# Optimization experiments

Measured on AMD Instinct MI355X. Metric: run time of the kernel, lower is better.

## Reference

```python
import jax, jax.numpy as jnp
import numpy as np

B, C, CI, H, W = 4, 128, 64, 96, 96  # batch, in_channels, inter_channels, spatial
SS = 2                                # sub_sample_factor (maxpool on phi and g)
BN_EPS = 1e-5


def conv1x1(x, w, b):
    # x: [B,C,H,W], w: [O,C], b: [O]
    return jnp.einsum('bchw,oc->bohw', x, w) + b[None, :, None, None]


def maxpool2(x):
    # 2x2 max pool, stride 2. x: [B,C,H,W]
    b, c, h, w = x.shape
    return x.reshape(b, c, h // 2, 2, w // 2, 2).max(axis=(3, 5))


def setup_inputs() -> dict:
    key = jax.random.key(0)
    ks = jax.random.split(key, 12)
    s_in = 1.0 / np.sqrt(C)
    s_ci = 1.0 / np.sqrt(CI)
    return {
        'x':        jax.random.normal(ks[0], (B, C, H, W), jnp.float32),
        'g_w':      jax.random.normal(ks[1], (CI, C), jnp.float32) * s_in,
        'g_b':      jax.random.normal(ks[2], (CI,), jnp.float32) * 0.01,
        'theta_w':  jax.random.normal(ks[3], (CI, C), jnp.float32) * s_in,
        'theta_b':  jax.random.normal(ks[4], (CI,), jnp.float32) * 0.01,
        'phi_w':    jax.random.normal(ks[5], (CI, C), jnp.float32) * s_in,
        'phi_b':    jax.random.normal(ks[6], (CI,), jnp.float32) * 0.01,
        'W_w':      jax.random.normal(ks[7], (C, CI), jnp.float32) * s_ci,
        'W_b':      jax.random.normal(ks[8], (C,), jnp.float32) * 0.01,
        'bn_gamma': jax.random.normal(ks[9], (C,), jnp.float32) * 0.1 + 1.0,
        'bn_beta':  jax.random.normal(ks[10], (C,), jnp.float32) * 0.1,
        'bn_mean':  jax.random.normal(ks[11], (C,), jnp.float32) * 0.1,
        'bn_var':   jax.random.uniform(jax.random.fold_in(key, 99), (C,), jnp.float32, 0.5, 1.5),
    }


def reference(x, g_w, g_b, theta_w, theta_b, phi_w, phi_b, W_w, W_b,
              bn_gamma, bn_beta, bn_mean, bn_var):
    b = x.shape[0]
    # g: conv1x1 -> maxpool(2) -> [B, N_kv, CI]
    g_x = maxpool2(conv1x1(x, g_w, g_b)).reshape(b, CI, -1).transpose(0, 2, 1)
    # theta: conv1x1 -> [B, N_q, CI]
    theta_x = conv1x1(x, theta_w, theta_b).reshape(b, CI, -1).transpose(0, 2, 1)
    # phi: conv1x1 -> maxpool(2) -> [B, CI, N_kv]
    phi_x = maxpool2(conv1x1(x, phi_w, phi_b)).reshape(b, CI, -1)
    # full affinity [B, N_q, N_kv], softmax over keys (embedded_gaussian)
    f = jnp.einsum('bqc,bck->bqk', theta_x, phi_x)
    attn = jax.nn.softmax(f, axis=-1)
    y = jnp.einsum('bqk,bkc->bqc', attn, g_x)            # [B, N_q, CI]
    y = y.transpose(0, 2, 1).reshape(b, CI, H, W)
    # W: conv1x1 (CI -> C) + BatchNorm (inference form) + residual
    W_y = conv1x1(y, W_w, W_b)
    inv = bn_gamma * jax.lax.rsqrt(bn_var + BN_EPS)
    W_y = W_y * inv[None, :, None, None] + (bn_beta - bn_mean * inv)[None, :, None, None]
    return W_y + x
```

## Files before the change

kernel.cpp:

```cpp
#include <hip/hip_runtime.h>
#include <hip/hip_bf16.h>

#define NB 4
#define NC 128
#define NH 96
#define NQ 9216
#define NKV 2304

typedef __bf16 bf8 __attribute__((ext_vector_type(8)));
typedef float f4 __attribute__((ext_vector_type(4)));
typedef unsigned short u16t;
typedef unsigned int u32t;
typedef u32t u32x4 __attribute__((ext_vector_type(4)));
typedef u16t u16x4v __attribute__((ext_vector_type(4)));

static __device__ __forceinline__ u16t f2bf(float f){
  u32t u = __builtin_bit_cast(u32t, f);
  u = (u + 0x7fffu + ((u >> 16) & 1u)) >> 16;
  return (u16t)u;
}
static __device__ __forceinline__ float bf2f(u16t h){
  return __builtin_bit_cast(float, ((u32t)h) << 16);
}

static __device__ __forceinline__ f4 mfma16(bf8 a, bf8 b, f4 c){
  return __builtin_amdgcn_mfma_f32_16x16x32_bf16(a, b, c, 0, 0, 0);
}

#define GLDS16(gp, lp) __builtin_amdgcn_global_load_lds( \
    (const u32t*)(gp), (u32t*)(lp), 16, 0, 0)

__global__ __launch_bounds__(256) void prep_weights(
    const float* __restrict__ g_w, const float* __restrict__ theta_w,
    const float* __restrict__ phi_w, const float* __restrict__ W_w,
    const float* __restrict__ W_b, const float* __restrict__ bn_gamma,
    const float* __restrict__ bn_beta, const float* __restrict__ bn_mean,
    const float* __restrict__ bn_var,
    u16t* __restrict__ wt_theta, u16t* __restrict__ wt_phi,
    u16t* __restrict__ wt_g, u16t* __restrict__ wt_W,
    float* __restrict__ alpha, float* __restrict__ beta2)
{
  int i = blockIdx.x * 256 + threadIdx.x;
  wt_theta[i] = f2bf(theta_w[i]);
  wt_phi[i]   = f2bf(phi_w[i]);
  wt_g[i]     = f2bf(g_w[i]);
  wt_W[i]     = f2bf(W_w[i]);
  if (blockIdx.x == 0 && threadIdx.x < 128){
    int t = threadIdx.x;
    float inv = bn_gamma[t] * rsqrtf(bn_var[t] + 1e-5f);
    alpha[t] = inv;
    beta2[t] = W_b[t]*inv + bn_beta[t] - bn_mean[t]*inv;
  }
}

__global__ __launch_bounds__(256) void conv3_pool(
    const float* __restrict__ x,
    const u16t* __restrict__ wt_theta, const u16t* __restrict__ wt_phi,
    const u16t* __restrict__ wt_g,
    const float* __restrict__ theta_b, const float* __restrict__ phi_b,
    const float* __restrict__ g_b,
    u16t* __restrict__ theta, u16t* __restrict__ phi, u16t* __restrict__ g_t)
{
  __shared__ __align__(16) u16t xt[64][136];
  const int blk = blockIdx.x;
  const int batch = blk / 144;
  const int t144 = blk % 144;
  const int ph = t144 / 3;
  const int pw0 = (t144 % 3) * 16;
  const int t = threadIdx.x;
  const float* xb = x + (size_t)batch * NC * NQ;

  #pragma unroll
  for (int i = 0; i < 8; ++i){
    int slot = i*256 + t;
    int c = slot >> 4;
    int quad = slot & 15;
    int row = quad >> 3, col4 = (quad & 7)*4;
    int q = (ph*2 + row)*NH + pw0*2 + col4;
    float4 v = *(const float4*)&xb[(size_t)c*NQ + q];
    int pl = row*32 + col4;
    u32t lo, hi;
    asm("v_cvt_pk_bf16_f32 %0, %1, %2" : "=v"(lo) : "v"(v.x), "v"(v.y));
    asm("v_cvt_pk_bf16_f32 %0, %1, %2" : "=v"(hi) : "v"(v.z), "v"(v.w));
    xt[pl+0][c] = (u16t)lo;
    xt[pl+1][c] = (u16t)(lo >> 16);
    xt[pl+2][c] = (u16t)hi;
    xt[pl+3][c] = (u16t)(hi >> 16);
  }
  __syncthreads();

  const int w = t >> 6, l = t & 63, lm = l & 15, lg = l >> 4;
  auto PL = [](int pxi){
    return (((pxi>>1)&1) << 5) + 8*(pxi>>4) + 2*((pxi>>2)&3) + (pxi&1);
  };
  auto QROW = [&](int pxi){
    return (ph*2 + ((pxi>>1)&1))*NH + (pw0 + 4*(pxi>>4) + ((pxi>>2)&3))*2 + (pxi&1);
  };
  bf8 a[4];
  #pragma unroll
  for (int k = 0; k < 4; ++k)
    a[k] = *(const bf8*)&xt[PL(w*16 + lm)][k*32 + lg*8];

  const int kvbase = ph*48 + pw0;
  const int kv = kvbase + 4*w + lg;

  f4 Dth[4];
  #pragma unroll
  for (int s = 0; s < 4; ++s){
    float bv = theta_b[s*16 + lm];
    f4 D = {bv, bv, bv, bv};
    #pragma unroll
    for (int k = 0; k < 4; ++k){
      bf8 b = *(const bf8*)&wt_theta[(s*16 + lm)*128 + k*32 + lg*8];
      D = mfma16(a[k], b, D);
    }
    Dth[s] = D;
  }
  {
    u16t* pp = phi + (size_t)batch * NKV * 64;
    #pragma unroll
    for (int s = 0; s < 4; ++s){
      float bv = phi_b[s*16 + lm];
      f4 D = {bv, bv, bv, bv};
      #pragma unroll
      for (int k = 0; k < 4; ++k){
        bf8 b = *(const bf8*)&wt_phi[(s*16 + lm)*128 + k*32 + lg*8];
        D = mfma16(a[k], b, D);
      }
      float mx = fmaxf(fmaxf(D[0], D[1]), fmaxf(D[2], D[3]));
      pp[(size_t)kv*64 + s*16 + lm] = f2bf(mx);
    }
  }
  float gmx[4];
  #pragma unroll
  for (int s = 0; s < 4; ++s){
    float bv = g_b[s*16 + lm];
    f4 D = {bv, bv, bv, bv};
    #pragma unroll
    for (int k = 0; k < 4; ++k){
      bf8 b = *(const bf8*)&wt_g[(s*16 + lm)*128 + k*32 + lg*8];
      D = mfma16(a[k], b, D);
    }
    gmx[s] = fmaxf(fmaxf(D[0], D[1]), fmaxf(D[2], D[3]));
  }

  __syncthreads();
  u16t* tl = &xt[0][0];
  u16t* gl = &xt[0][0] + 4608;
  #pragma unroll
  for (int s = 0; s < 4; ++s){
    #pragma unroll
    for (int r = 0; r < 4; ++r)
      tl[(w*16 + lg*4 + r)*72 + s*16 + lm] = f2bf(Dth[s][r]);
    gl[(s*16 + lm)*20 + 4*w + lg] = f2bf(gmx[s]);
  }
  __syncthreads();
  {
    u16t* th = theta + (size_t)batch * NQ * 64;
    #pragma unroll
    for (int p = 0; p < 2; ++p){
      int slot = t + 256*p;
      int row = slot >> 3, piece = slot & 7;
      int q = QROW(row);
      *(bf8*)&th[(size_t)q*64 + piece*8] = *(const bf8*)&tl[row*72 + piece*8];
    }
  }
  {
    u16t* gt = g_t + (size_t)batch * 64 * NKV;
    int c = t >> 2, L = t & 3;
    int T = (kvbase >> 4) & 3;
    int kvg = kvbase & ~63;
    u16x4v v;
    #pragma unroll
    for (int u = 0; u < 4; ++u) v[u] = gl[c*20 + L*4 + u];
    *(u16x4v*)&gt[(size_t)c*NKV + kvg + (T>>1)*32 + ((T&1)<<2) + L*8] = v;
  }
}


__global__ __launch_bounds__(256) void attn_partial(
    const u16t* __restrict__ theta, const u16t* __restrict__ phi,
    const u16t* __restrict__ g_t,
    u16t* __restrict__ yp_ws, float* __restrict__ sums_ws)
{
  __shared__ __align__(16) char SM[32768];

  const int bid = blockIdx.x;
  const int blkL = (bid & 7)*96 + (bid >> 3);
  const int batch = blkL / 192;
  const int rem = blkL % 192;
  const int qb = (rem >> 1) * 96;
  const int khb = rem & 1;
  const int t = threadIdx.x;
  const int w = t >> 6, l = t & 63, lm = l & 15, lg = l >> 4;
  const int qw = w >> 1, khw = w & 1;

  const u16t* th = theta + ((size_t)batch*NQ + qb)*64;
  bf8 a[3][2];
  #pragma unroll
  for (int mr = 0; mr < 3; ++mr){
    a[mr][0] = *(const bf8*)&th[(qw*48 + mr*16 + lm)*64 + lg*8];
    a[mr][1] = *(const bf8*)&th[(qw*48 + mr*16 + lm)*64 + 32 + lg*8];
  }
  asm volatile("s_waitcnt vmcnt(0)" ::: "memory");

  const char* phc = (const char*)(phi + (size_t)batch*NKV*64);
  const char* gtc = (const char*)(g_t + (size_t)batch*64*NKV);

  auto STAGE = [&](int kt_s, int bufc){
    #pragma unroll
    for (int j = 0; j < 4; ++j){
      int u = w*4 + j;
      int khu = u >> 3, isg = (u >> 2) & 1, sub = u & 3;
      int kb = khb*1152 + khu*576 + kt_s*32;
      char* dst;
      const char* src;
      if (!isg){
        int row = sub*8 + (l >> 3);
        int swz = ((l & 7) ^ (l >> 3)) << 4;
        dst = SM + (khu*2 + bufc)*4096 + sub*1024 + l*16;
        src = phc + (size_t)(kb + row)*128 + swz;
      } else {
        int row = sub*16 + (l >> 2);
        int swz = (((l & 3) ^ ((l >> 2) & 3)) << 4);
        dst = SM + 16384 + (khu*2 + bufc)*4096 + sub*1024 + l*16;
        src = gtc + (size_t)row*(NKV*2) + (size_t)kb*2 + swz;
      }
      GLDS16(src, dst);
    }
  };

  f4 Y[3][4];
  #pragma unroll
  for (int mr = 0; mr < 3; ++mr)
    #pragma unroll
    for (int s = 0; s < 4; ++s)
      Y[mr][s] = f4{0.f, 0.f, 0.f, 0.f};
  float lsum[3] = {0.f, 0.f, 0.f};

  STAGE(0, 0);

  for (int kt = 0; kt < 18; ++kt){
    const int buf = kt & 1;
    __builtin_amdgcn_s_barrier();
    asm volatile("" ::: "memory");
    if (kt < 17){
      STAGE(kt + 1, buf ^ 1);
      asm volatile("s_waitcnt vmcnt(4)" ::: "memory");
    } else {
      asm volatile("s_waitcnt vmcnt(0)" ::: "memory");
    }
    __builtin_amdgcn_s_barrier();
    asm volatile("" ::: "memory");
    __builtin_amdgcn_sched_barrier(0);

    __builtin_amdgcn_s_setprio(1);

    const char* pb = SM + (khw*2 + buf)*4096;
    const char* gb = SM + 16384 + (khw*2 + buf)*4096;
    const int m7 = lm & 7;

    bf8 bp[2][2];
    #pragma unroll
    for (int tt = 0; tt < 2; ++tt){
      int rb = (tt*16 + lm)*128;
      bp[tt][0] = *(const bf8*)(pb + rb + ((lg ^ m7) << 4));
      bp[tt][1] = *(const bf8*)(pb + rb + (((4 + lg) ^ m7) << 4));
    }
    bf8 bg[4];
    #pragma unroll
    for (int s = 0; s < 4; ++s){
      int rb = (s*16 + lm)*64;
      bg[s] = *(const bf8*)(gb + rb + ((lg ^ (lm & 3)) << 4));
    }

    #pragma unroll
    for (int mr = 0; mr < 3; ++mr){
      f4 S[2];
      #pragma unroll
      for (int tt = 0; tt < 2; ++tt){
        f4 z = {0.f, 0.f, 0.f, 0.f};
        z = mfma16(bp[tt][0], a[mr][0], z);
        S[tt] = mfma16(bp[tt][1], a[mr][1], z);
      }
      u32t wq[4];
      #pragma unroll
      for (int tt = 0; tt < 2; ++tt){
        float p0, p1, p2, p3;
        float a0 = fmaf(S[tt][0], 1.44269504f, -43.2808512f);
        float a1 = fmaf(S[tt][1], 1.44269504f, -43.2808512f);
        float a2 = fmaf(S[tt][2], 1.44269504f, -43.2808512f);
        float a3 = fmaf(S[tt][3], 1.44269504f, -43.2808512f);
        asm("v_exp_f32 %0, %1" : "=v"(p0) : "v"(a0));
        asm("v_exp_f32 %0, %1" : "=v"(p1) : "v"(a1));
        asm("v_exp_f32 %0, %1" : "=v"(p2) : "v"(a2));
        asm("v_exp_f32 %0, %1" : "=v"(p3) : "v"(a3));
        lsum[mr] += (p0 + p1) + (p2 + p3);
        asm("v_cvt_pk_bf16_f32 %0, %1, %2" : "=v"(wq[tt*2])   : "v"(p0), "v"(p1));
        asm("v_cvt_pk_bf16_f32 %0, %1, %2" : "=v"(wq[tt*2+1]) : "v"(p2), "v"(p3));
      }
      bf8 pa = __builtin_bit_cast(bf8, u32x4{wq[0], wq[1], wq[2], wq[3]});
      #pragma unroll
      for (int s = 0; s < 4; ++s)
        Y[mr][s] = mfma16(pa, bg[s], Y[mr][s]);
    }
    __builtin_amdgcn_s_setprio(0);
  }

  float sv[3];
  #pragma unroll
  for (int mr = 0; mr < 3; ++mr){
    float s0 = lsum[mr];
    s0 += __shfl_xor(s0, 16);
    s0 += __shfl_xor(s0, 32);
    sv[mr] = s0;
  }

  __syncthreads();
  float (*ypL)[68] = (float (*)[68])SM;
  if (khw == 0){
    #pragma unroll
    for (int mr = 0; mr < 3; ++mr){
      #pragma unroll
      for (int s = 0; s < 4; ++s)
        #pragma unroll
        for (int r = 0; r < 4; ++r)
          ypL[qw*48 + mr*16 + lg*4 + r][s*16 + lm] = Y[mr][s][r];
      if (lg == 0)
        ypL[qw*48 + mr*16 + lm][64] = sv[mr];
    }
  }
  __syncthreads();
  if (khw == 1){
    #pragma unroll
    for (int mr = 0; mr < 3; ++mr){
      #pragma unroll
      for (int s = 0; s < 4; ++s)
        #pragma unroll
        for (int r = 0; r < 4; ++r)
          ypL[qw*48 + mr*16 + lg*4 + r][s*16 + lm] += Y[mr][s][r];
      if (lg == 0)
        ypL[qw*48 + mr*16 + lm][64] += sv[mr];
    }
  }
  __syncthreads();

  u16t* ypg = yp_ws + (size_t)blkL * (96*64);
  float* sg  = sums_ws + (size_t)blkL * 96;
  #pragma unroll
  for (int i = 0; i < 6; ++i){
    int idx = t + 256*i;
    int q = idx >> 4, c4 = (idx & 15)*4;
    u16x4v v;
    #pragma unroll
    for (int j = 0; j < 4; ++j) v[j] = f2bf(ypL[q][c4 + j]);
    *(u16x4v*)&ypg[q*64 + c4] = v;
  }
  if (t < 96) sg[t] = ypL[t][64];
}

__global__ __launch_bounds__(256) void combine_out(
    const u16t* __restrict__ yp_ws, const float* __restrict__ sums_ws,
    const u16t* __restrict__ wt_W,
    const float* __restrict__ alpha, const float* __restrict__ beta2,
    const float* __restrict__ x, float* __restrict__ out)
{
  __shared__ __align__(16) u16t yl[96][72];
  __shared__ __align__(16) float ol[96][131];
  const int bid = blockIdx.x;
  const int blk = (bid & 7)*48 + (bid >> 3);
  const int batch = blk / 96;
  const int qg = blk % 96;
  const int qb = qg * 96;
  const int t = threadIdx.x;
  const int w = t >> 6, l = t & 63, lm = l & 15, lg = l >> 4;

  const u16t* pA = yp_ws + ((size_t)batch*192 + qg*2) * (96*64);
  const u16t* pB = pA + 96*64;
  const float* sA = sums_ws + ((size_t)batch*192 + qg*2) * 96;
  const float* sB = sA + 96;

  #pragma unroll
  for (int i = 0; i < 6; ++i){
    int idx = t + 256*i;
    int q = idx >> 4, c4 = (idx & 15)*4;
    float inv = 1.0f / (sA[q] + sB[q]);
    u16x4v a4 = *(const u16x4v*)&pA[q*64 + c4];
    u16x4v b4 = *(const u16x4v*)&pB[q*64 + c4];
    u16x4v v;
    #pragma unroll
    for (int j = 0; j < 4; ++j)
      v[j] = f2bf((bf2f(a4[j]) + bf2f(b4[j])) * inv);
    *(u16x4v*)&yl[q][c4] = v;
  }
  __syncthreads();

  #pragma unroll
  for (int i = 0; i < 12; ++i){
    int tau = w + 4*i;
    int qt = tau >> 3, ct = tau & 7;
    bf8 ya0 = *(const bf8*)&yl[qt*16 + lm][lg*8];
    bf8 ya1 = *(const bf8*)&yl[qt*16 + lm][32 + lg*8];
    const u16t* wr = wt_W + (ct*16 + lm)*64;
    bf8 b0 = *(const bf8*)&wr[lg*8];
    bf8 b1 = *(const bf8*)&wr[lg*8 + 32];
    f4 z = {0.f, 0.f, 0.f, 0.f};
    z = mfma16(ya0, b0, z);
    z = mfma16(ya1, b1, z);
    #pragma unroll
    for (int r = 0; r < 4; ++r)
      ol[qt*16 + lg*4 + r][ct*16 + lm] = z[r];
  }
  __syncthreads();

  const float* xb = x + (size_t)batch*NC*NQ + qb;
  float* ob = out + (size_t)batch*NC*NQ + qb;
  #pragma unroll
  for (int i = 0; i < 12; ++i){
    int idx = t + 256*i;
    int c = idx / 24, qv = idx % 24;
    float4 xv = *(const float4*)&xb[(size_t)c*NQ + qv*4];
    float al = alpha[c], be = beta2[c];
    float4 ov;
    ov.x = ol[qv*4 + 0][c]*al + be + xv.x;
    ov.y = ol[qv*4 + 1][c]*al + be + xv.y;
    ov.z = ol[qv*4 + 2][c]*al + be + xv.z;
    ov.w = ol[qv*4 + 3][c]*al + be + xv.w;
    *(float4*)&ob[(size_t)c*NQ + qv*4] = ov;
  }
}

extern "C" void kernel_launch(void* const* d_in, const int* in_sizes, int n_in,
                              void* d_out, int out_size, void* d_ws, size_t ws_size,
                              hipStream_t stream)
{
  const float* x       = (const float*)d_in[0];
  const float* g_w     = (const float*)d_in[1];
  const float* g_b     = (const float*)d_in[2];
  const float* theta_w = (const float*)d_in[3];
  const float* theta_b = (const float*)d_in[4];
  const float* phi_w   = (const float*)d_in[5];
  const float* phi_b   = (const float*)d_in[6];
  const float* W_w     = (const float*)d_in[7];
  const float* W_b     = (const float*)d_in[8];
  const float* bn_g    = (const float*)d_in[9];
  const float* bn_b    = (const float*)d_in[10];
  const float* bn_m    = (const float*)d_in[11];
  const float* bn_v    = (const float*)d_in[12];
  float* out = (float*)d_out;

  char* ws = (char*)d_ws;
  size_t off = 0;
  u16t* theta = (u16t*)(ws + off); off += (size_t)NB*NQ*64*2;
  u16t* phi   = (u16t*)(ws + off); off += (size_t)NB*NKV*64*2;
  u16t* g_t   = (u16t*)(ws + off); off += (size_t)NB*64*NKV*2;
  u16t* wt_theta = (u16t*)(ws + off); off += 64*128*2;
  u16t* wt_phi   = (u16t*)(ws + off); off += 64*128*2;
  u16t* wt_g     = (u16t*)(ws + off); off += 64*128*2;
  u16t* wt_W     = (u16t*)(ws + off); off += 128*64*2;
  float* alpha = (float*)(ws + off); off += 128*4;
  float* beta2 = (float*)(ws + off); off += 128*4;
  u16t* yp_ws  = (u16t*)(ws + off); off += (size_t)768*96*64*2;
  float* sums_ws = (float*)(ws + off); off += (size_t)768*96*4;
  if (off > ws_size) return;

  prep_weights<<<32, 256, 0, stream>>>(g_w, theta_w, phi_w, W_w, W_b,
                                       bn_g, bn_b, bn_m, bn_v,
                                       wt_theta, wt_phi, wt_g, wt_W, alpha, beta2);
  conv3_pool<<<576, 256, 0, stream>>>(x, wt_theta, wt_phi, wt_g,
                                      theta_b, phi_b, g_b, theta, phi, g_t);
  attn_partial<<<768, 256, 0, stream>>>(theta, phi, g_t, yp_ws, sums_ws);
  combine_out<<<384, 256, 0, stream>>>(yp_ws, sums_ws, wt_W, alpha, beta2, x, out);
}
```

Measured before the change: 73.59 us.

## Replace block-shared double-buffered KV staging with per-wave private buffers

Each wave now loads its own phi and g tiles into a private LDS region every iteration, so the two block-wide barriers per key tile go away. Within an iteration the QK^T and exp work runs while the g tile is still loading, and the PV MFMAs are reordered to loop over g fragments on the outside. In exchange, the prefetch of the next tile across iterations is lost. Waves that share the same key half now each fetch the same data, which doubles global/L2 load traffic.

```diff
diff --git a/kernel.cpp b/kernel.cpp
--- a/kernel.cpp
+++ b/kernel.cpp
@@ -206,29 +206,8 @@
 
   const char* phc = (const char*)(phi + (size_t)batch*NKV*64);
   const char* gtc = (const char*)(g_t + (size_t)batch*64*NKV);
-
-  auto STAGE = [&](int kt_s, int bufc){
-    #pragma unroll
-    for (int j = 0; j < 4; ++j){
-      int u = w*4 + j;
-      int khu = u >> 3, isg = (u >> 2) & 1, sub = u & 3;
-      int kb = khb*1152 + khu*576 + kt_s*32;
-      char* dst;
-      const char* src;
-      if (!isg){
-        int row = sub*8 + (l >> 3);
-        int swz = ((l & 7) ^ (l >> 3)) << 4;
-        dst = SM + (khu*2 + bufc)*4096 + sub*1024 + l*16;
-        src = phc + (size_t)(kb + row)*128 + swz;
-      } else {
-        int row = sub*16 + (l >> 2);
-        int swz = (((l & 3) ^ ((l >> 2) & 3)) << 4);
-        dst = SM + 16384 + (khu*2 + bufc)*4096 + sub*1024 + l*16;
-        src = gtc + (size_t)row*(NKV*2) + (size_t)kb*2 + swz;
-      }
-      GLDS16(src, dst);
-    }
-  };
+  char* const pbuf = SM + w*8192;
+  char* const gbuf = pbuf + 4096;
 
   f4 Y[3][4];
   #pragma unroll
@@ -238,42 +217,35 @@
       Y[mr][s] = f4{0.f, 0.f, 0.f, 0.f};
   float lsum[3] = {0.f, 0.f, 0.f};
 
-  STAGE(0, 0);
+  const int m7 = lm & 7;
 
   for (int kt = 0; kt < 18; ++kt){
-    const int buf = kt & 1;
-    __builtin_amdgcn_s_barrier();
-    asm volatile("" ::: "memory");
-    if (kt < 17){
-      STAGE(kt + 1, buf ^ 1);
-      asm volatile("s_waitcnt vmcnt(4)" ::: "memory");
-    } else {
-      asm volatile("s_waitcnt vmcnt(0)" ::: "memory");
-    }
-    __builtin_amdgcn_s_barrier();
-    asm volatile("" ::: "memory");
+    const int kb = khb*1152 + khw*576 + kt*32;
+    #pragma unroll
+    for (int sub = 0; sub < 4; ++sub){
+      int row = sub*8 + (l >> 3);
+      int swz = ((l & 7) ^ (l >> 3)) << 4;
+      GLDS16(phc + (size_t)(kb + row)*128 + swz, pbuf + sub*1024 + l*16);
+    }
+    #pragma unroll
+    for (int sub = 0; sub < 4; ++sub){
+      int row = sub*16 + (l >> 2);
+      int swz = (((l & 3) ^ ((l >> 2) & 3)) << 4);
+      GLDS16(gtc + (size_t)row*(NKV*2) + (size_t)kb*2 + swz,
+             gbuf + sub*1024 + l*16);
+    }
+    asm volatile("s_waitcnt vmcnt(4)" ::: "memory");
     __builtin_amdgcn_sched_barrier(0);
-
     __builtin_amdgcn_s_setprio(1);
-
-    const char* pb = SM + (khw*2 + buf)*4096;
-    const char* gb = SM + 16384 + (khw*2 + buf)*4096;
-    const int m7 = lm & 7;
 
     bf8 bp[2][2];
     #pragma unroll
     for (int tt = 0; tt < 2; ++tt){
       int rb = (tt*16 + lm)*128;
-      bp[tt][0] = *(const bf8*)(pb + rb + ((lg ^ m7) << 4));
-      bp[tt][1] = *(const bf8*)(pb + rb + (((4 + lg) ^ m7) << 4));
-    }
-    bf8 bg[4];
-    #pragma unroll
-    for (int s = 0; s < 4; ++s){
-      int rb = (s*16 + lm)*64;
-      bg[s] = *(const bf8*)(gb + rb + ((lg ^ (lm & 3)) << 4));
-    }
-
+      bp[tt][0] = *(const bf8*)(pbuf + rb + ((lg ^ m7) << 4));
+      bp[tt][1] = *(const bf8*)(pbuf + rb + (((4 + lg) ^ m7) << 4));
+    }
+    bf8 pa[3];
     #pragma unroll
     for (int mr = 0; mr < 3; ++mr){
       f4 S[2];
@@ -299,11 +271,24 @@
         asm("v_cvt_pk_bf16_f32 %0, %1, %2" : "=v"(wq[tt*2])   : "v"(p0), "v"(p1));
         asm("v_cvt_pk_bf16_f32 %0, %1, %2" : "=v"(wq[tt*2+1]) : "v"(p2), "v"(p3));
       }
-      bf8 pa = __builtin_bit_cast(bf8, u32x4{wq[0], wq[1], wq[2], wq[3]});
-      #pragma unroll
-      for (int s = 0; s < 4; ++s)
-        Y[mr][s] = mfma16(pa, bg[s], Y[mr][s]);
-    }
+      pa[mr] = __builtin_bit_cast(bf8, u32x4{wq[0], wq[1], wq[2], wq[3]});
+    }
+    __builtin_amdgcn_s_setprio(0);
+
+    asm volatile("s_waitcnt vmcnt(0)" ::: "memory");
+    __builtin_amdgcn_sched_barrier(0);
+    __builtin_amdgcn_s_setprio(1);
+    bf8 bg[4];
+    #pragma unroll
+    for (int s = 0; s < 4; ++s){
+      int rb = (s*16 + lm)*64;
+      bg[s] = *(const bf8*)(gbuf + rb + ((lg ^ (lm & 3)) << 4));
+    }
+    #pragma unroll
+    for (int s = 0; s < 4; ++s)
+      #pragma unroll
+      for (int mr = 0; mr < 3; ++mr)
+        Y[mr][s] = mfma16(pa[mr], bg[s], Y[mr][s]);
     __builtin_amdgcn_s_setprio(0);
   }
 
```

After: 78.54 us, median of 2. 6.7% more time.
